# Optimization experiments

Measured on AMD Instinct MI355X. Metric: run time of the kernel, lower is better.

Reference implementation:

```python
import jax, jax.numpy as jnp
import numpy as np

NEG_RATIO = 5          # neg_sample_ratio, also k (num_nodes-1 >> ratio)
THRESH = 0.7           # hard_neg_threshold
SMOOTH = 0.1           # label_smoothing
NUM_NODES = 200_000
DIM = 128
B = 1024               # batch size, all labels == 1 (all positives)
FILL_VAL = -1.0e9


def _l2_normalize(x, eps=1e-12):
    # F.normalize(p=2, dim=-1): divide by clamped L2 norm
    n = jnp.sqrt(jnp.sum(x * x, axis=-1, keepdims=True))
    return x / jnp.maximum(n, eps)


def setup_inputs() -> dict:
    key = jax.random.key(0)
    k1, k2, k3, k4 = jax.random.split(key, 4)
    src_nodes = jax.random.randint(k1, (B,), 0, NUM_NODES)
    dst_nodes = jax.random.randint(k2, (B,), 0, NUM_NODES)
    labels = jnp.ones((B,), dtype=jnp.float32)  # all positives -> pos_mask all True
    timestamps = jax.random.uniform(k3, (B,), dtype=jnp.float32)
    memory = jax.random.normal(k4, (NUM_NODES, DIM), dtype=jnp.float32)
    return {
        "src_nodes": src_nodes,
        "dst_nodes": dst_nodes,
        "labels": labels,
        "timestamps": timestamps,
        "memory": memory,
    }


def reference(src_nodes, dst_nodes, labels, timestamps, memory):
    # --- embedding gather + L2 normalize ---
    src_emb = memory[src_nodes]                      # [B, D]
    s = _l2_normalize(src_emb).astype(jnp.float16)   # use_half_precision=True
    c = _l2_normalize(memory).astype(jnp.float16)    # [N, D]

    # --- similarity [B, N], back to fp32 ---
    sim = jnp.matmul(s, c.T).astype(jnp.float32)

    # --- mask out ground-truth dst and below-threshold sims ---
    cols = jnp.arange(NUM_NODES)
    allowed = cols[None, :] != dst_nodes[:, None]    # exclude GT positives
    valid = allowed & (sim > THRESH)
    score = jnp.where(valid, sim, FILL_VAL)

    # --- top-k hard negatives per positive ---
    k = NEG_RATIO  # min(neg_sample_ratio, num_nodes-1)
    topk_vals, topk_idx = jax.lax.top_k(score, k)    # [B, k]
    is_real = (topk_vals > FILL_VAL + 1.0).reshape(-1)  # [B*k]

    # --- fallback random negatives (fixed-shape equivalent of the torch
    #     pack-real-then-pad-random assembly; total count == B*k either way) ---
    rkey = jax.random.key(42)
    rand_dst = jax.random.randint(rkey, (B * k,), 0, NUM_NODES)
    src_rep = jnp.repeat(src_nodes, k)               # [B*k]
    rand_dst = jnp.where(rand_dst == src_rep, (rand_dst + 1) % NUM_NODES, rand_dst)

    final_src = src_rep
    final_dst = jnp.where(is_real, topk_idx.reshape(-1), rand_dst)
    neg_ts = jnp.repeat(timestamps, k)

    # --- assemble augmented batch ---
    new_src = jnp.concatenate([src_nodes, final_src])
    new_dst = jnp.concatenate([dst_nodes, final_dst])
    new_labels = jnp.concatenate([labels, jnp.zeros((B * k,), labels.dtype)])
    new_ts = jnp.concatenate([timestamps, neg_ts])

    # --- label smoothing ---
    new_labels = new_labels * (1.0 - SMOOTH) + (1.0 - new_labels) * SMOOTH

    return new_src, new_dst, new_labels, new_ts, topk_vals
```

## Files before the change

kernel.cpp:

```cpp
#include <hip/hip_runtime.h>

#define NUM_NODES 200000
#define DIM 128
#define BATCH 1024
#define K_NEG 5
#define CAP 16
#define JW 64
#define BN (4 * JW)
#define THRESH 0.7f
#define FILL (-1.0e9f)

typedef __attribute__((ext_vector_type(8))) short short8;
typedef __attribute__((ext_vector_type(16))) float f32x16;

__device__ __forceinline__ unsigned short f2bf(float x) {
  unsigned u = __builtin_bit_cast(unsigned, x);
  return (unsigned short)((u + 0x7fffu + ((u >> 16) & 1u)) >> 16);
}

__device__ __forceinline__ void tf2x32(unsigned k0, unsigned k1,
                                       unsigned x0, unsigned x1,
                                       unsigned* o0, unsigned* o1) {
  unsigned ks2 = k0 ^ k1 ^ 0x1BD11BDAu;
  unsigned v0 = x0 + k0, v1 = x1 + k1;
#define TFR(r) { v0 += v1; v1 = (v1 << r) | (v1 >> (32 - r)); v1 ^= v0; }
  TFR(13) TFR(15) TFR(26) TFR(6)   v0 += k1;  v1 += ks2 + 1u;
  TFR(17) TFR(29) TFR(16) TFR(24)  v0 += ks2; v1 += k0 + 2u;
  TFR(13) TFR(15) TFR(26) TFR(6)   v0 += k0;  v1 += k1 + 3u;
  TFR(17) TFR(29) TFR(16) TFR(24)  v0 += k1;  v1 += ks2 + 4u;
  TFR(13) TFR(15) TFR(26) TFR(6)   v0 += ks2; v1 += k0 + 5u;
#undef TFR
  *o0 = v0; *o1 = v1;
}

__device__ __forceinline__ unsigned rbits32(unsigned ka, unsigned kb, unsigned m) {
  unsigned o0, o1;
  tf2x32(ka, kb, 0u, m, &o0, &o1);
  return o0 ^ o1;
}

__global__ void prep_kernel(const float* __restrict__ memory,
                            const int* __restrict__ src_nodes,
                            unsigned short* __restrict__ s16f,
                            int* __restrict__ cand_cnt) {
  int tid = threadIdx.x;
  int gid = blockIdx.x * 256 + tid;
  if (gid < BATCH) cand_cnt[gid] = 0;
  int row = blockIdx.x * 4 + (tid >> 6);
  int L = tid & 63;
  int s = src_nodes[row];
  float2 v = ((const float2*)(memory + (size_t)s * DIM))[L];
  float ss = v.x * v.x + v.y * v.y;
#pragma unroll
  for (int off = 32; off > 0; off >>= 1) ss += __shfl_xor(ss, off);
  float inv = 1.0f / fmaxf(sqrtf(ss), 1e-12f);
  unsigned p = (unsigned)f2bf(v.x * inv) | ((unsigned)f2bf(v.y * inv) << 16);
  int ms = row >> 5, l32 = row & 31;
  int c = L >> 2;
  int ks = c >> 1, half = c & 1;
  ((unsigned*)s16f)[(((ms * 8 + ks) * 64) + half * 32 + l32) * 4 + (L & 3)] = p;
}

__global__ __launch_bounds__(256, 2) void sim_scan_kernel(
    const float* __restrict__ memory,
    const unsigned short* __restrict__ s16f,
    const int* __restrict__ dst_nodes,
    int* __restrict__ cand_cnt,
    float* __restrict__ cand_val,
    int* __restrict__ cand_idx) {
  __shared__ short8 aT[4096];
  int tid = threadIdx.x;
  int wid = tid >> 6;
  int lane = tid & 63;
  int half = lane >> 5;
  int l32 = lane & 31;
  int jb = blockIdx.x * BN + wid * JW;

  short8 bf[2][8];
#pragma unroll
  for (int js = 0; js < 2; ++js) {
    int j = jb + js * 32 + l32;
    bool jv = (j < NUM_NODES);
    const float4* rp4 = (const float4*)(memory + (size_t)j * DIM);
    float4 q[16];
#pragma unroll
    for (int ks = 0; ks < 8; ++ks) {
      q[ks * 2]     = jv ? rp4[ks * 4 + half * 2]     : make_float4(0.f, 0.f, 0.f, 0.f);
      q[ks * 2 + 1] = jv ? rp4[ks * 4 + half * 2 + 1] : make_float4(0.f, 0.f, 0.f, 0.f);
    }
    float ss = 0.0f;
#pragma unroll
    for (int i = 0; i < 16; ++i)
      ss += q[i].x * q[i].x + q[i].y * q[i].y + q[i].z * q[i].z + q[i].w * q[i].w;
    ss += __shfl_xor(ss, 32);
    float inv = 1.0f / fmaxf(sqrtf(ss), 1e-12f);
#pragma unroll
    for (int ks = 0; ks < 8; ++ks) {
      float4 a = q[ks * 2], b = q[ks * 2 + 1];
      short8 f;
      f[0] = (short)f2bf(a.x * inv); f[1] = (short)f2bf(a.y * inv);
      f[2] = (short)f2bf(a.z * inv); f[3] = (short)f2bf(a.w * inv);
      f[4] = (short)f2bf(b.x * inv); f[5] = (short)f2bf(b.y * inv);
      f[6] = (short)f2bf(b.z * inv); f[7] = (short)f2bf(b.w * inv);
      bf[js][ks] = f;
    }
  }

  const short8* __restrict__ afg = (const short8*)s16f;

  for (int p = 0; p < 4; ++p) {
    __syncthreads();
#pragma unroll
    for (int c = 0; c < 16; ++c) {
      int idx = c * 256 + tid;
      aT[idx] = afg[p * 4096 + idx];
    }
    __syncthreads();

#pragma unroll
    for (int ml = 0; ml < 8; ++ml) {
      int ms = p * 8 + ml;
      short8 a[8];
#pragma unroll
      for (int ks = 0; ks < 8; ++ks) a[ks] = aT[(ml * 8 + ks) * 64 + lane];
      f32x16 acc0, acc1;
#pragma unroll
      for (int i = 0; i < 16; ++i) { acc0[i] = 0.0f; acc1[i] = 0.0f; }
#pragma unroll
      for (int ks = 0; ks < 8; ++ks) {
        acc0 = __builtin_amdgcn_mfma_f32_32x32x16_bf16(a[ks], bf[0][ks], acc0, 0, 0, 0);
        acc1 = __builtin_amdgcn_mfma_f32_32x32x16_bf16(a[ks], bf[1][ks], acc1, 0, 0, 0);
      }
      float m[16];
#pragma unroll
      for (int i = 0; i < 16; ++i) m[i] = fmaxf(acc0[i], acc1[i]);
#pragma unroll
      for (int i = 0; i < 8; ++i) m[i] = fmaxf(m[i], m[i + 8]);
#pragma unroll
      for (int i = 0; i < 4; ++i) m[i] = fmaxf(m[i], m[i + 4]);
      float vm = fmaxf(fmaxf(m[0], m[1]), fmaxf(m[2], m[3]));
      if (vm > THRESH) {
#pragma unroll
        for (int js = 0; js < 2; ++js) {
          int gj = jb + js * 32 + l32;
#pragma unroll
          for (int r = 0; r < 16; ++r) {
            float v = (js == 0) ? acc0[r] : acc1[r];
            if (v > THRESH) {
              int gi = ms * 32 + (r & 3) + 8 * (r >> 2) + 4 * half;
              if (gj < NUM_NODES && gj != dst_nodes[gi]) {
                int pp = atomicAdd(&cand_cnt[gi], 1);
                if (pp < CAP) {
                  cand_val[gi * CAP + pp] = v;
                  cand_idx[gi * CAP + pp] = gj;
                }
              }
            }
          }
        }
      }
    }
  }
}

__global__ void finalize_kernel(const int* __restrict__ src_nodes,
                                const int* __restrict__ dst_nodes,
                                const float* __restrict__ labels,
                                const float* __restrict__ ts,
                                const int* __restrict__ cand_cnt,
                                const float* __restrict__ cand_val,
                                const int* __restrict__ cand_idx,
                                float* __restrict__ out) {
  int r = blockIdx.x * 256 + threadIdx.x;
  if (r >= BATCH) return;
  const int TOT = BATCH + BATCH * K_NEG;
  int srcv = src_nodes[r];
  float tsv = ts[r];
  out[r] = (float)srcv;
  out[TOT + r] = (float)dst_nodes[r];
  float l = labels[r];
  out[2 * TOT + r] = l * 0.9f + (1.0f - l) * 0.1f;
  out[3 * TOT + r] = tsv;

  int cnt = cand_cnt[r];
  cnt = cnt < CAP ? cnt : CAP;
  float cv[CAP]; int ci[CAP];
  for (int i = 0; i < cnt; ++i) { cv[i] = cand_val[r * CAP + i]; ci[i] = cand_idx[r * CAP + i]; }

  unsigned k1a, k1b, k2a, k2b;
  tf2x32(0u, 42u, 0u, 0u, &k1a, &k1b);
  tf2x32(0u, 42u, 0u, 1u, &k2a, &k2b);

  const unsigned span = 200000u;
  const unsigned mult = 167296u;

  for (int s = 0; s < K_NEG; ++s) {
    int sel = -1;
    for (int i = 0; i < cnt; ++i)
      if (sel < 0 || cv[i] > cv[sel] || (cv[i] == cv[sel] && ci[i] < ci[sel])) sel = i;
    float v = FILL; int idx = 0;
    if (sel >= 0) { v = cv[sel]; idx = ci[sel]; cv[sel] = FILL; ci[sel] = 0x7fffffff; }
    bool is_real = v > (FILL + 1.0f);

    unsigned m = (unsigned)(r * K_NEG + s);
    unsigned hi = rbits32(k1a, k1b, m);
    unsigned lo = rbits32(k2a, k2b, m);
    unsigned off = ((hi % span) * mult + (lo % span)) % span;
    int rd = (int)off;
    if (rd == srcv) rd = (rd + 1) % NUM_NODES;
    int fd = is_real ? idx : rd;

    int mi = (int)m;
    out[BATCH + mi] = (float)srcv;
    out[TOT + BATCH + mi] = (float)fd;
    out[2 * TOT + BATCH + mi] = 0.1f;
    out[3 * TOT + BATCH + mi] = tsv;
    out[4 * TOT + mi] = v;
  }
}

extern "C" void kernel_launch(void* const* d_in, const int* in_sizes, int n_in,
                              void* d_out, int out_size, void* d_ws, size_t ws_size,
                              hipStream_t stream) {
  const int* src = (const int*)d_in[0];
  const int* dst = (const int*)d_in[1];
  const float* labels = (const float*)d_in[2];
  const float* ts = (const float*)d_in[3];
  const float* memory = (const float*)d_in[4];
  float* out = (float*)d_out;

  char* ws = (char*)d_ws;
  unsigned short* s16f = (unsigned short*)ws;
  int* cand_cnt = (int*)(ws + 262144);
  float* cand_val = (float*)(ws + 266240);
  int* cand_idx = (int*)(ws + 331776);

  prep_kernel<<<256, 256, 0, stream>>>(memory, src, s16f, cand_cnt);
  int jblocks = (NUM_NODES + BN - 1) / BN;
  sim_scan_kernel<<<jblocks, 256, 0, stream>>>(memory, s16f, dst, cand_cnt, cand_val, cand_idx);
  finalize_kernel<<<(BATCH + 255) / 256, 256, 0, stream>>>(src, dst, labels, ts,
                                                           cand_cnt, cand_val, cand_idx, out);
}
```

Baseline: 229.2 us.

## Switch similarity matmul to FP8 MFMA with a separate candidate-prep kernel

Normalized query and candidate embeddings are quantized to FP8 (e4m3-style, software-encoded) instead of bf16, and the matmul uses 32x32x16 fp8 MFMA, halving the A-tile LDS footprint and raising launch bounds occupancy to 4 blocks. Candidate normalization and quantization move into a separate prep_c kernel that writes fragment-ordered FP8 data to workspace, which the scan kernel then reads directly. The costs are an extra kernel launch, a round trip of the quantized candidate matrix through global memory, and reduced precision near the 0.7 threshold, which can change which candidates pass the threshold and their order in the top-k.

```diff
diff --git a/kernel.cpp b/kernel.cpp
--- a/kernel.cpp
+++ b/kernel.cpp
@@ -7,15 +7,26 @@
 #define CAP 16
 #define JW 64
 #define BN (4 * JW)
+#define JBLOCKS 782
 #define THRESH 0.7f
 #define FILL (-1.0e9f)
 
-typedef __attribute__((ext_vector_type(8))) short short8;
 typedef __attribute__((ext_vector_type(16))) float f32x16;
 
-__device__ __forceinline__ unsigned short f2bf(float x) {
+__device__ __forceinline__ unsigned char f2fp8(float x) {
   unsigned u = __builtin_bit_cast(unsigned, x);
-  return (unsigned short)((u + 0x7fffu + ((u >> 16) & 1u)) >> 16);
+  unsigned char s = (unsigned char)((u >> 24) & 0x80u);
+  float ax = fabsf(x);
+  unsigned char enc;
+  if (ax < 0.015625f) {
+    enc = (unsigned char)(int)rintf(ax * 512.0f);
+  } else {
+    int ee; float fr = frexpf(ax, &ee);
+    int E = ee + 6;
+    int mant = (int)rintf((fr * 2.0f - 1.0f) * 8.0f);
+    enc = (unsigned char)((E << 3) + mant);
+  }
+  return (unsigned char)(enc | s);
 }
 
 __device__ __forceinline__ void tf2x32(unsigned k0, unsigned k1,
@@ -39,10 +50,11 @@
   return o0 ^ o1;
 }
 
-__global__ void prep_kernel(const float* __restrict__ memory,
-                            const int* __restrict__ src_nodes,
-                            unsigned short* __restrict__ s16f,
-                            int* __restrict__ cand_cnt) {
+
+__global__ void prep_a_kernel(const float* __restrict__ memory,
+                              const int* __restrict__ src_nodes,
+                              unsigned char* __restrict__ afragA,
+                              int* __restrict__ cand_cnt) {
   int tid = threadIdx.x;
   int gid = blockIdx.x * 256 + tid;
   if (gid < BATCH) cand_cnt[gid] = 0;
@@ -54,21 +66,65 @@
 #pragma unroll
   for (int off = 32; off > 0; off >>= 1) ss += __shfl_xor(ss, off);
   float inv = 1.0f / fmaxf(sqrtf(ss), 1e-12f);
-  unsigned p = (unsigned)f2bf(v.x * inv) | ((unsigned)f2bf(v.y * inv) << 16);
+  unsigned char b0 = f2fp8(v.x * inv), b1 = f2fp8(v.y * inv);
   int ms = row >> 5, l32 = row & 31;
-  int c = L >> 2;
-  int ks = c >> 1, half = c & 1;
-  ((unsigned*)s16f)[(((ms * 8 + ks) * 64) + half * 32 + l32) * 4 + (L & 3)] = p;
-}
-
-__global__ __launch_bounds__(256, 2) void sim_scan_kernel(
-    const float* __restrict__ memory,
-    const unsigned short* __restrict__ s16f,
+  int c = 2 * L;
+  int kp = c >> 5, half = (c >> 3) & 1, tp = ((c >> 4) & 1) * 8 + (c & 7);
+  size_t chunk = ((size_t)(ms * 4 + kp)) * 64 + half * 32 + l32;
+  *(unsigned short*)(afragA + chunk * 16 + tp) =
+      (unsigned short)((unsigned)b0 | ((unsigned)b1 << 8));
+}
+
+__global__ void prep_c_kernel(const float* __restrict__ memory,
+                              unsigned long long* __restrict__ cfrag) {
+  int tid = threadIdx.x;
+  int wid = tid >> 6;
+  int lane = tid & 63;
+  int half = lane >> 5;
+  int l32 = lane & 31;
+  int rowbase = blockIdx.x * BN + wid * 64;
+#pragma unroll
+  for (int js = 0; js < 2; ++js) {
+    int j = rowbase + js * 32 + l32;
+    bool jv = (j < NUM_NODES);
+    const float4* rp4 = (const float4*)(memory + (size_t)j * DIM);
+    float4 q[16];
+#pragma unroll
+    for (int ks = 0; ks < 8; ++ks) {
+      q[ks * 2]     = jv ? rp4[ks * 4 + half * 2]     : make_float4(0.f, 0.f, 0.f, 0.f);
+      q[ks * 2 + 1] = jv ? rp4[ks * 4 + half * 2 + 1] : make_float4(0.f, 0.f, 0.f, 0.f);
+    }
+    float ss = 0.0f;
+#pragma unroll
+    for (int i = 0; i < 16; ++i)
+      ss += q[i].x * q[i].x + q[i].y * q[i].y + q[i].z * q[i].z + q[i].w * q[i].w;
+    ss += __shfl_xor(ss, 32);
+    float inv = 1.0f / fmaxf(sqrtf(ss), 1e-12f);
+#pragma unroll
+    for (int ks = 0; ks < 8; ++ks) {
+      float4 a = q[ks * 2], b = q[ks * 2 + 1];
+      unsigned long long w =
+          (unsigned long long)f2fp8(a.x * inv)
+        | ((unsigned long long)f2fp8(a.y * inv) << 8)
+        | ((unsigned long long)f2fp8(a.z * inv) << 16)
+        | ((unsigned long long)f2fp8(a.w * inv) << 24)
+        | ((unsigned long long)f2fp8(b.x * inv) << 32)
+        | ((unsigned long long)f2fp8(b.y * inv) << 40)
+        | ((unsigned long long)f2fp8(b.z * inv) << 48)
+        | ((unsigned long long)f2fp8(b.w * inv) << 56);
+      cfrag[((size_t)(j >> 5) * 8 + ks) * 64 + half * 32 + l32] = w;
+    }
+  }
+}
+
+__global__ __launch_bounds__(256, 4) void sim_scan_kernel(
+    const ulong2* __restrict__ afragG,
+    const unsigned long long* __restrict__ cfrag,
     const int* __restrict__ dst_nodes,
     int* __restrict__ cand_cnt,
     float* __restrict__ cand_val,
     int* __restrict__ cand_idx) {
-  __shared__ short8 aT[4096];
+  __shared__ ulong2 aT[2048];
   int tid = threadIdx.x;
   int wid = tid >> 6;
   int lane = tid & 63;
@@ -76,60 +132,40 @@
   int l32 = lane & 31;
   int jb = blockIdx.x * BN + wid * JW;
 
-  short8 bf[2][8];
-#pragma unroll
-  for (int js = 0; js < 2; ++js) {
-    int j = jb + js * 32 + l32;
-    bool jv = (j < NUM_NODES);
-    const float4* rp4 = (const float4*)(memory + (size_t)j * DIM);
-    float4 q[16];
-#pragma unroll
-    for (int ks = 0; ks < 8; ++ks) {
-      q[ks * 2]     = jv ? rp4[ks * 4 + half * 2]     : make_float4(0.f, 0.f, 0.f, 0.f);
-      q[ks * 2 + 1] = jv ? rp4[ks * 4 + half * 2 + 1] : make_float4(0.f, 0.f, 0.f, 0.f);
-    }
-    float ss = 0.0f;
-#pragma unroll
-    for (int i = 0; i < 16; ++i)
-      ss += q[i].x * q[i].x + q[i].y * q[i].y + q[i].z * q[i].z + q[i].w * q[i].w;
-    ss += __shfl_xor(ss, 32);
-    float inv = 1.0f / fmaxf(sqrtf(ss), 1e-12f);
-#pragma unroll
-    for (int ks = 0; ks < 8; ++ks) {
-      float4 a = q[ks * 2], b = q[ks * 2 + 1];
-      short8 f;
-      f[0] = (short)f2bf(a.x * inv); f[1] = (short)f2bf(a.y * inv);
-      f[2] = (short)f2bf(a.z * inv); f[3] = (short)f2bf(a.w * inv);
-      f[4] = (short)f2bf(b.x * inv); f[5] = (short)f2bf(b.y * inv);
-      f[6] = (short)f2bf(b.z * inv); f[7] = (short)f2bf(b.w * inv);
-      bf[js][ks] = f;
-    }
-  }
-
-  const short8* __restrict__ afg = (const short8*)s16f;
+  long bf[2][8];
+#pragma unroll
+  for (int js = 0; js < 2; ++js)
+#pragma unroll
+    for (int ks = 0; ks < 8; ++ks)
+      bf[js][ks] = (long)cfrag[((size_t)((jb >> 5) + js) * 8 + ks) * 64 + lane];
 
   for (int p = 0; p < 4; ++p) {
     __syncthreads();
-#pragma unroll
-    for (int c = 0; c < 16; ++c) {
+    const ulong2* g = afragG + p * 2048;
+#pragma unroll
+    for (int c = 0; c < 8; ++c) {
       int idx = c * 256 + tid;
-      aT[idx] = afg[p * 4096 + idx];
+      aT[idx] = g[idx];
     }
     __syncthreads();
 
 #pragma unroll
     for (int ml = 0; ml < 8; ++ml) {
       int ms = p * 8 + ml;
-      short8 a[8];
-#pragma unroll
-      for (int ks = 0; ks < 8; ++ks) a[ks] = aT[(ml * 8 + ks) * 64 + lane];
+      ulong2 av[4];
+#pragma unroll
+      for (int kp = 0; kp < 4; ++kp) av[kp] = aT[(ml * 4 + kp) * 64 + lane];
       f32x16 acc0, acc1;
 #pragma unroll
       for (int i = 0; i < 16; ++i) { acc0[i] = 0.0f; acc1[i] = 0.0f; }
 #pragma unroll
-      for (int ks = 0; ks < 8; ++ks) {
-        acc0 = __builtin_amdgcn_mfma_f32_32x32x16_bf16(a[ks], bf[0][ks], acc0, 0, 0, 0);
-        acc1 = __builtin_amdgcn_mfma_f32_32x32x16_bf16(a[ks], bf[1][ks], acc1, 0, 0, 0);
+      for (int kp = 0; kp < 4; ++kp) {
+        long alo = (long)av[kp].x;
+        long ahi = (long)av[kp].y;
+        acc0 = __builtin_amdgcn_mfma_f32_32x32x16_fp8_fp8(alo, bf[0][2 * kp], acc0, 0, 0, 0);
+        acc1 = __builtin_amdgcn_mfma_f32_32x32x16_fp8_fp8(alo, bf[1][2 * kp], acc1, 0, 0, 0);
+        acc0 = __builtin_amdgcn_mfma_f32_32x32x16_fp8_fp8(ahi, bf[0][2 * kp + 1], acc0, 0, 0, 0);
+        acc1 = __builtin_amdgcn_mfma_f32_32x32x16_fp8_fp8(ahi, bf[1][2 * kp + 1], acc1, 0, 0, 0);
       }
       float m[16];
 #pragma unroll
@@ -230,14 +266,17 @@
   float* out = (float*)d_out;
 
   char* ws = (char*)d_ws;
-  unsigned short* s16f = (unsigned short*)ws;
-  int* cand_cnt = (int*)(ws + 262144);
-  float* cand_val = (float*)(ws + 266240);
-  int* cand_idx = (int*)(ws + 331776);
-
-  prep_kernel<<<256, 256, 0, stream>>>(memory, src, s16f, cand_cnt);
-  int jblocks = (NUM_NODES + BN - 1) / BN;
-  sim_scan_kernel<<<jblocks, 256, 0, stream>>>(memory, s16f, dst, cand_cnt, cand_val, cand_idx);
+  unsigned long long* cfrag = (unsigned long long*)ws;
+  size_t off = (size_t)JBLOCKS * 256 * 128;
+  unsigned char* afragA = (unsigned char*)(ws + off);
+  int* cand_cnt = (int*)(ws + off + 131072);
+  float* cand_val = (float*)(ws + off + 135168);
+  int* cand_idx = (int*)(ws + off + 200704);
+
+  prep_a_kernel<<<256, 256, 0, stream>>>(memory, src, afragA, cand_cnt);
+  prep_c_kernel<<<JBLOCKS, 256, 0, stream>>>(memory, cfrag);
+  sim_scan_kernel<<<JBLOCKS, 256, 0, stream>>>((const ulong2*)afragA, cfrag, dst,
+                                               cand_cnt, cand_val, cand_idx);
   finalize_kernel<<<(BATCH + 255) / 256, 256, 0, stream>>>(src, dst, labels, ts,
                                                            cand_cnt, cand_val, cand_idx, out);
 }
```

After: 227.0 us. About the same (-0.9%).
